# Optimization experiments

Measured on AMD Instinct MI355X. Metric: run time of the kernel, lower is better.

The kernel has to match this reference:

```python
import jax, jax.numpy as jnp
import numpy as np

FFT_LEN = 64
BATCH = 262144  # large batch -> memory-bound; per-sample math is a tiny 64x64 DFT
PILOT_IDX = np.array([11, 25, 39, 53])


def _dft_kernels():
    # Exact replication of ComplexIFFT.__init__: cos/sin DFT matrices scaled by 1/N.
    n = np.arange(FFT_LEN).reshape(-1, 1)
    k = np.arange(FFT_LEN)
    cos_k = (np.cos(2.0 * np.pi * k * n / FFT_LEN) / FFT_LEN).astype(np.float32)
    sin_k = (np.sin(2.0 * np.pi * k * n / FFT_LEN) / FFT_LEN).astype(np.float32)
    return jnp.asarray(cos_k), jnp.asarray(sin_k)


def setup_inputs() -> dict:
    key = jax.random.key(0)
    eq_freq = jax.random.normal(key, (BATCH, 2, FFT_LEN), dtype=jnp.float32)
    cos_kernel, sin_kernel = _dft_kernels()
    return {"eq_freq": eq_freq, "cos_kernel": cos_kernel, "sin_kernel": sin_kernel}


def reference(eq_freq, cos_kernel, sin_kernel):
    # insert_pilots: set subcarriers 11/25/39/53 to (1.0 + 0.0j) on every batch row.
    idx = jnp.asarray(PILOT_IDX)
    x = eq_freq.at[:, 0, idx].set(1.0).at[:, 1, idx].set(0.0)  # (B, 2, 64)

    x_real = x[:, 0, :]  # (B, 64)
    x_imag = x[:, 1, :]

    # conv1d(1->64, kernel=64) on a length-64 signal == matmul with the 64x64 kernel:
    # out[b, n] = sum_k kernel[n, k] * x[b, k]
    rr = jnp.einsum('bk,nk->bn', x_real, cos_kernel)
    ri = jnp.einsum('bk,nk->bn', x_imag, cos_kernel)
    ir = jnp.einsum('bk,nk->bn', x_real, sin_kernel)
    ii = jnp.einsum('bk,nk->bn', x_imag, sin_kernel)

    out_real = rr - ii  # (B, 64)
    out_imag = ri + ir

    # torch: permute to (B, 64->len, 1) then cat on dim=1 -> (B, 2, 64) after squeeze semantics;
    # concretely out_real/out_imag each become (B, 1, 64) and are concatenated on dim 1.
    return jnp.stack([out_real, out_imag], axis=1)  # (B, 2, 64)
```

## Files before the change

### kernel.cpp

```cpp
#include <hip/hip_runtime.h>
#include <hip/hip_bf16.h>

typedef __attribute__((ext_vector_type(8))) short short8;
typedef __attribute__((ext_vector_type(4))) float float4v;

#define LDSROW 136

static __device__ inline short f2bf(float f) {
    union { float f; unsigned u; } v; v.f = f;
    unsigned u = v.u;
    u += 0x7fffu + ((u >> 16) & 1u);
    return (short)(u >> 16);
}

__global__ __launch_bounds__(256, 4)
void ofdm_idft_kernel(const float* __restrict__ eq,
                      const float* __restrict__ cosk,
                      const float* __restrict__ sink,
                      float* __restrict__ out)
{
    __shared__ short Wt[128 * LDSROW];

    const int tid = threadIdx.x;

    for (int idx = tid; idx < 128 * 128; idx += 256) {
        const int n = idx >> 7;
        const int k = idx & 127;
        const int nn = n & 63, km = k & 63;
        float v;
        if (n < 64) {
            v = (k < 64) ? cosk[n * 64 + k] : -sink[n * 64 + km];
        } else {
            v = (k < 64) ? sink[nn * 64 + k] : cosk[nn * 64 + km];
        }
        Wt[n * LDSROW + k] = f2bf(v);
    }
    __syncthreads();

    const int lane = tid & 63;
    const int wave = tid >> 6;
    const int m    = lane & 15;
    const int q    = lane >> 4;

    const unsigned long long PMASK =
        (1ull << 11) | (1ull << 25) | (1ull << 39) | (1ull << 53);

    const int wave_id = blockIdx.x * 4 + wave;

    for (int t = 0; t < 4; ++t) {
        const int b0 = wave_id * 64 + t * 16;
        const float* arow = eq + (size_t)(b0 + m) * 128;

        short8 afrag[4];
        #pragma unroll
        for (int kk = 0; kk < 4; ++kk) {
            const int kbase = kk * 32 + q * 8;
            const float4v x0 = *(const float4v*)(arow + kbase);
            const float4v x1 = *(const float4v*)(arow + kbase + 4);
            short8 f;
            #pragma unroll
            for (int j = 0; j < 8; ++j) {
                float xv = (j < 4) ? x0[j] : x1[j - 4];
                const int k = kbase + j;
                if ((PMASK >> (k & 63)) & 1ull)
                    xv = (k < 64) ? 1.0f : 0.0f;
                f[j] = f2bf(xv);
            }
            afrag[kk] = f;
        }

        float4v acc[8];
        #pragma unroll
        for (int nt = 0; nt < 8; ++nt) acc[nt] = (float4v){0.f, 0.f, 0.f, 0.f};

        #pragma unroll
        for (int kk = 0; kk < 4; ++kk) {
            #pragma unroll
            for (int nt = 0; nt < 8; ++nt) {
                const short8 bfrag =
                    *(const short8*)&Wt[(nt * 16 + m) * LDSROW + kk * 32 + q * 8];
                acc[nt] = __builtin_amdgcn_mfma_f32_16x16x32_bf16(
                    afrag[kk], bfrag, acc[nt], 0, 0, 0);
            }
        }

        float* orow = out + (size_t)b0 * 128;
        #pragma unroll
        for (int nt = 0; nt < 8; ++nt) {
            #pragma unroll
            for (int r = 0; r < 4; ++r) {
                orow[(size_t)(q * 4 + r) * 128 + nt * 16 + m] = acc[nt][r];
            }
        }
    }
}

extern "C" void kernel_launch(void* const* d_in, const int* in_sizes, int n_in,
                              void* d_out, int out_size, void* d_ws, size_t ws_size,
                              hipStream_t stream) {
    const float* eq   = (const float*)d_in[0];
    const float* cosk = (const float*)d_in[1];
    const float* sink = (const float*)d_in[2];
    float* out = (float*)d_out;
    hipLaunchKernelGGL(ofdm_idft_kernel, dim3(1024), dim3(256), 0, stream,
                       eq, cosk, sink, out);
}
```

Measured before the change: 294.1 us.

## Precompute bf16 DFT matrix in separate kernel, read B-fragments from global/L2

Moves construction of the combined 128x128 bf16 DFT weight matrix into a small pre-kernel that writes to the workspace. The main kernel no longer stages weights in LDS and drops its block-wide sync; each wave handles 32 rows as two 16-row tiles, loading all inputs up front and reusing each B-fragment across both tiles. The grid doubles and the occupancy hint drops. In exchange, every wave reloads the weights from L2/global instead of LDS, and there is an extra kernel launch.

```diff
diff --git a/kernel.cpp b/kernel.cpp
--- a/kernel.cpp
+++ b/kernel.cpp
@@ -1,10 +1,7 @@
 #include <hip/hip_runtime.h>
-#include <hip/hip_bf16.h>
 
 typedef __attribute__((ext_vector_type(8))) short short8;
 typedef __attribute__((ext_vector_type(4))) float float4v;
-
-#define LDSROW 136
 
 static __device__ inline short f2bf(float f) {
     union { float f; unsigned u; } v; v.f = f;
@@ -13,85 +10,93 @@
     return (short)(u >> 16);
 }
 
-__global__ __launch_bounds__(256, 4)
+__global__ __launch_bounds__(256)
+void build_wt(const float* __restrict__ cosk, const float* __restrict__ sink,
+              short* __restrict__ wt)
+{
+    const int idx = blockIdx.x * 256 + threadIdx.x;
+    const int n = idx >> 7, k = idx & 127;
+    const int nn = n & 63, km = k & 63;
+    float v;
+    if (n < 64) v = (k < 64) ? cosk[n * 64 + k] : -sink[n * 64 + km];
+    else        v = (k < 64) ? sink[nn * 64 + k] : cosk[nn * 64 + km];
+    wt[idx] = f2bf(v);
+}
+
+__global__ __launch_bounds__(256, 2)
 void ofdm_idft_kernel(const float* __restrict__ eq,
-                      const float* __restrict__ cosk,
-                      const float* __restrict__ sink,
+                      const short* __restrict__ wt,
                       float* __restrict__ out)
 {
-    __shared__ short Wt[128 * LDSROW];
-
-    const int tid = threadIdx.x;
-
-    for (int idx = tid; idx < 128 * 128; idx += 256) {
-        const int n = idx >> 7;
-        const int k = idx & 127;
-        const int nn = n & 63, km = k & 63;
-        float v;
-        if (n < 64) {
-            v = (k < 64) ? cosk[n * 64 + k] : -sink[n * 64 + km];
-        } else {
-            v = (k < 64) ? sink[nn * 64 + k] : cosk[nn * 64 + km];
-        }
-        Wt[n * LDSROW + k] = f2bf(v);
-    }
-    __syncthreads();
-
-    const int lane = tid & 63;
-    const int wave = tid >> 6;
-    const int m    = lane & 15;
-    const int q    = lane >> 4;
+    const int lane = threadIdx.x & 63;
+    const int wave = threadIdx.x >> 6;
+    const int m = lane & 15;
+    const int q = lane >> 4;
+    const int b0 = (blockIdx.x * 4 + wave) * 32;
 
     const unsigned long long PMASK =
         (1ull << 11) | (1ull << 25) | (1ull << 39) | (1ull << 53);
 
-    const int wave_id = blockIdx.x * 4 + wave;
-
-    for (int t = 0; t < 4; ++t) {
-        const int b0 = wave_id * 64 + t * 16;
-        const float* arow = eq + (size_t)(b0 + m) * 128;
-
-        short8 afrag[4];
+    float4v x[16];
+    const float* a0 = eq + (size_t)(b0 + m) * 128 + q * 8;
+    #pragma unroll
+    for (int u = 0; u < 2; ++u) {
+        const float* a = a0 + u * (16 * 128);
         #pragma unroll
         for (int kk = 0; kk < 4; ++kk) {
-            const int kbase = kk * 32 + q * 8;
-            const float4v x0 = *(const float4v*)(arow + kbase);
-            const float4v x1 = *(const float4v*)(arow + kbase + 4);
+            x[u * 8 + kk * 2 + 0] = *(const float4v*)(a + kk * 32);
+            x[u * 8 + kk * 2 + 1] = *(const float4v*)(a + kk * 32 + 4);
+        }
+    }
+
+    short8 afr[2][4];
+    #pragma unroll
+    for (int u = 0; u < 2; ++u) {
+        #pragma unroll
+        for (int kk = 0; kk < 4; ++kk) {
             short8 f;
             #pragma unroll
             for (int j = 0; j < 8; ++j) {
-                float xv = (j < 4) ? x0[j] : x1[j - 4];
-                const int k = kbase + j;
+                float xv = (j < 4) ? x[u * 8 + kk * 2][j] : x[u * 8 + kk * 2 + 1][j - 4];
+                const int k = kk * 32 + q * 8 + j;
                 if ((PMASK >> (k & 63)) & 1ull)
                     xv = (k < 64) ? 1.0f : 0.0f;
                 f[j] = f2bf(xv);
             }
-            afrag[kk] = f;
+            afr[u][kk] = f;
         }
+    }
 
-        float4v acc[8];
+    float4v acc[2][8];
+    #pragma unroll
+    for (int u = 0; u < 2; ++u)
         #pragma unroll
-        for (int nt = 0; nt < 8; ++nt) acc[nt] = (float4v){0.f, 0.f, 0.f, 0.f};
+        for (int nt = 0; nt < 8; ++nt)
+            acc[u][nt] = (float4v){0.f, 0.f, 0.f, 0.f};
 
+    #pragma unroll
+    for (int kk = 0; kk < 4; ++kk) {
+        short8 bfr[8];
         #pragma unroll
-        for (int kk = 0; kk < 4; ++kk) {
-            #pragma unroll
-            for (int nt = 0; nt < 8; ++nt) {
-                const short8 bfrag =
-                    *(const short8*)&Wt[(nt * 16 + m) * LDSROW + kk * 32 + q * 8];
-                acc[nt] = __builtin_amdgcn_mfma_f32_16x16x32_bf16(
-                    afrag[kk], bfrag, acc[nt], 0, 0, 0);
-            }
-        }
-
-        float* orow = out + (size_t)b0 * 128;
+        for (int nt = 0; nt < 8; ++nt)
+            bfr[nt] = *(const short8*)(wt + (nt * 16 + m) * 128 + kk * 32 + q * 8);
         #pragma unroll
         for (int nt = 0; nt < 8; ++nt) {
+            acc[0][nt] = __builtin_amdgcn_mfma_f32_16x16x32_bf16(
+                afr[0][kk], bfr[nt], acc[0][nt], 0, 0, 0);
+            acc[1][nt] = __builtin_amdgcn_mfma_f32_16x16x32_bf16(
+                afr[1][kk], bfr[nt], acc[1][nt], 0, 0, 0);
+        }
+    }
+
+    #pragma unroll
+    for (int u = 0; u < 2; ++u) {
+        float* orow = out + (size_t)(b0 + u * 16) * 128;
+        #pragma unroll
+        for (int r = 0; r < 4; ++r)
             #pragma unroll
-            for (int r = 0; r < 4; ++r) {
-                orow[(size_t)(q * 4 + r) * 128 + nt * 16 + m] = acc[nt][r];
-            }
-        }
+            for (int nt = 0; nt < 8; ++nt)
+                orow[(size_t)(q * 4 + r) * 128 + nt * 16 + m] = acc[u][nt][r];
     }
 }
 
@@ -102,6 +107,9 @@
     const float* cosk = (const float*)d_in[1];
     const float* sink = (const float*)d_in[2];
     float* out = (float*)d_out;
-    hipLaunchKernelGGL(ofdm_idft_kernel, dim3(1024), dim3(256), 0, stream,
-                       eq, cosk, sink, out);
+    short* wt  = (short*)d_ws;
+
+    hipLaunchKernelGGL(build_wt, dim3(64), dim3(256), 0, stream, cosk, sink, wt);
+    hipLaunchKernelGGL(ofdm_idft_kernel, dim3(2048), dim3(256), 0, stream,
+                       eq, wt, out);
 }
```

After: 257.4 us. 1.14x faster.
